# Kernel tuning notes

Measured on AMD Instinct MI355X. Metric: run time of the kernel, lower is better.

The kernel has to match this reference:

```python
import jax, jax.numpy as jnp
import numpy as np

SR = 48000.0
HARMONIC_NUM = 8
DIM = HARMONIC_NUM + 1
SINE_AMP = 0.1
NOISE_STD = 0.003
VOICED_THRESHOLD = 0.0


def setup_inputs() -> dict:
    key = jax.random.key(0)
    k1, k2, k3, k4 = jax.random.split(key, 4)
    B, L, upp = 4, 1000, 512
    Lo = L * upp
    f0 = jax.random.uniform(k1, (B, L), dtype=jnp.float32, minval=80.0, maxval=400.0)
    voiced = jax.random.uniform(k2, (B, L)) > 0.2
    f0 = f0 * voiced.astype(jnp.float32)
    rand_ini = jax.random.uniform(k3, (B, DIM), dtype=jnp.float32)
    noise_randn = jax.random.normal(k4, (B, Lo, DIM), dtype=jnp.float32)
    return {"f0": f0, "rand_ini": rand_ini, "noise_randn": noise_randn, "upp": upp}


def _linear_upsample_align_corners(x, upp):
    # x: (B, L, D) -> (B, L*upp, D), matches F.interpolate(mode='linear', align_corners=True)
    B, L, D = x.shape
    Lo = L * upp
    pos = jnp.arange(Lo, dtype=jnp.float32) * (jnp.float32(L - 1) / jnp.float32(Lo - 1))
    i0 = jnp.clip(jnp.floor(pos).astype(jnp.int32), 0, L - 2)
    frac = (pos - i0.astype(jnp.float32))[None, :, None]
    return x[:, i0, :] * (1.0 - frac) + x[:, i0 + 1, :] * frac


def reference(f0, rand_ini, noise_randn, upp):
    B, L = f0.shape
    Lo = L * upp
    # harmonics: f0, 2*f0, ..., DIM*f0  -> (B, L, DIM)
    f0_buf = f0[:, :, None] * jnp.arange(1, DIM + 1, dtype=f0.dtype)
    rad_values = (f0_buf / SR) % 1.0
    # random initial phase, first harmonic fixed at 0
    ri = rand_ini.at[:, 0].set(0.0)
    rad_values = rad_values.at[:, 0, :].add(ri)
    # cumulative phase at frame rate, scaled and upsampled
    tmp_over_one = jnp.cumsum(rad_values, axis=1) * upp
    tmp_over_one = _linear_upsample_align_corners(tmp_over_one, upp)  # (B, Lo, DIM)
    rad_up = jnp.repeat(rad_values, upp, axis=1)  # nearest upsample (B, Lo, DIM)
    tmp_over_one = tmp_over_one % 1.0
    # detect wrap-around and inject -1 phase shift so cumsum stays consistent
    wrap = (tmp_over_one[:, 1:, :] - tmp_over_one[:, :-1, :]) < 0
    cumsum_shift = jnp.concatenate(
        [jnp.zeros((B, 1, DIM), dtype=f0.dtype), -wrap.astype(f0.dtype)], axis=1
    )
    phase = jnp.cumsum(rad_up + cumsum_shift, axis=1)
    sine_waves = jnp.sin(phase * (2.0 * jnp.pi)) * SINE_AMP
    # voiced/unvoiced mask at frame rate, nearest-upsampled
    uv = (f0 > VOICED_THRESHOLD).astype(f0.dtype)[:, :, None]  # (B, L, 1)
    uv = jnp.repeat(uv, upp, axis=1)  # (B, Lo, 1)
    noise_amp = uv * NOISE_STD + (1.0 - uv) * (SINE_AMP / 3.0)
    noise = noise_amp * noise_randn
    sine_waves = sine_waves * uv + noise
    return sine_waves, uv, noise
```

## Files before the change

### kernel.cpp

```cpp
#include <hip/hip_runtime.h>
#include <math.h>

#define DIM 9
#define SINE_AMP 0.1f
#define NOISE_STD 0.003f

__global__ void __launch_bounds__(64)
phase_scan_kernel(const float* __restrict__ f0,
                  const float* __restrict__ rand_ini,
                  float* __restrict__ rad_out,
                  float* __restrict__ base_out,
                  int B, int L, int upp)
{
    const int bd   = blockIdx.x;
    const int b    = bd / DIM;
    const int d    = bd - b * DIM;
    const int lane = threadIdx.x;
    const float hf = (float)(d + 1);
    const float ri = (d == 0) ? 0.0f : rand_ini[b * DIM + d];

    double carry = 0.0;
    for (int c0 = 0; c0 < L; c0 += 64) {
        const int l = c0 + lane;
        float r = 0.0f;
        if (l < L) {
            float fb = f0[b * L + l] * hf;
            r = fmodf(fb / 48000.0f, 1.0f);
            if (l == 0) r += ri;
        }
        const double rd = (double)r;
        double inc = rd;
        #pragma unroll
        for (int off = 1; off < 64; off <<= 1) {
            double t = __shfl_up(inc, off, 64);
            if (lane >= off) inc += t;
        }
        if (l < L) {
            const double excl = carry + (inc - rd);
            double bf = excl * (double)upp;
            bf -= floor(bf);
            const int idx = (b * L + l) * DIM + d;
            rad_out[idx]  = r;
            base_out[idx] = (float)bf;
        }
        carry += __shfl(inc, 63, 64);
    }
}

template <int UPP>
__global__ void __launch_bounds__(256)
sine_gen_kernel(const float* __restrict__ f0,
                const float* __restrict__ noise_randn,
                const float* __restrict__ rad_arr,
                const float* __restrict__ base_arr,
                float* __restrict__ out_sine,
                float* __restrict__ out_uv,
                float* __restrict__ out_noise,
                int L, int Lo, int upp)
{
    const int b   = blockIdx.y;
    const int LoD = Lo * DIM;
    const int n4  = LoD >> 2;
    const long long boff = (long long)b * LoD;

    const float* __restrict__ nz_b    = noise_randn + boff;
    float* __restrict__       sine_b  = out_sine + boff;
    float* __restrict__       noise_b = out_noise + boff;
    const float* __restrict__ f0_b    = f0 + b * L;
    float* __restrict__       uv_b    = out_uv + (long long)b * Lo;
    const int fbase = b * L * DIM;

    for (int i4 = blockIdx.x * blockDim.x + threadIdx.x; i4 < n4;
         i4 += gridDim.x * blockDim.x) {
        const int i0 = i4 << 2;
        const float4 nr = *(const float4*)(nz_b + i0);
        const float nrk[4] = {nr.x, nr.y, nr.z, nr.w};
        float sv[4], nv[4];
        #pragma unroll
        for (int k = 0; k < 4; ++k) {
            const int rem = i0 + k;
            const int o = rem / DIM;
            const int d = rem - o * DIM;
            int l, j;
            if (UPP > 0) { l = o / UPP; j = o - l * UPP; }
            else         { l = o / upp; j = o - l * upp; }
            const int fidx = fbase + l * DIM + d;
            const float rad  = rad_arr[fidx];
            const float base = base_arr[fidx];
            float ph = base + (float)(j + 1) * rad;
            ph -= floorf(ph);
            float s;
            asm("v_sin_f32 %0, %1" : "=v"(s) : "v"(ph));
            const float f0v  = f0_b[l];
            const float uvf  = (f0v > 0.0f) ? 1.0f : 0.0f;
            const float namp = uvf * NOISE_STD + (1.0f - uvf) * (SINE_AMP / 3.0f);
            const float nzv  = namp * nrk[k];
            nv[k] = nzv;
            sv[k] = s * SINE_AMP * uvf + nzv;
            if (d == 0) uv_b[o] = uvf;
        }
        *(float4*)(sine_b + i0)  = make_float4(sv[0], sv[1], sv[2], sv[3]);
        *(float4*)(noise_b + i0) = make_float4(nv[0], nv[1], nv[2], nv[3]);
    }

    if (blockIdx.x == 0 && threadIdx.x < (LoD & 3)) {
        const int rem = (n4 << 2) + threadIdx.x;
        const int o = rem / DIM;
        const int d = rem - o * DIM;
        int l, j;
        if (UPP > 0) { l = o / UPP; j = o - l * UPP; }
        else         { l = o / upp; j = o - l * upp; }
        const int fidx = fbase + l * DIM + d;
        float ph = base_arr[fidx] + (float)(j + 1) * rad_arr[fidx];
        ph -= floorf(ph);
        float s;
        asm("v_sin_f32 %0, %1" : "=v"(s) : "v"(ph));
        const float f0v  = f0_b[l];
        const float uvf  = (f0v > 0.0f) ? 1.0f : 0.0f;
        const float namp = uvf * NOISE_STD + (1.0f - uvf) * (SINE_AMP / 3.0f);
        const float nzv  = namp * nz_b[rem];
        noise_b[rem] = nzv;
        sine_b[rem]  = s * SINE_AMP * uvf + nzv;
        if (d == 0) uv_b[o] = uvf;
    }
}

extern "C" void kernel_launch(void* const* d_in, const int* in_sizes, int n_in,
                              void* d_out, int out_size, void* d_ws, size_t ws_size,
                              hipStream_t stream)
{
    const float* f0       = (const float*)d_in[0];
    const float* rand_ini = (const float*)d_in[1];
    const float* noise    = (const float*)d_in[2];
    const int B  = in_sizes[1] / DIM;
    const int L  = in_sizes[0] / B;
    const int Lo = in_sizes[2] / (B * DIM);
    const int upp = Lo / L;

    float* out       = (float*)d_out;
    float* out_sine  = out;
    float* out_uv    = out_sine + (long long)B * Lo * DIM;
    float* out_noise = out_uv + (long long)B * Lo;

    float* rad_ws  = (float*)d_ws;
    float* base_ws = rad_ws + (size_t)B * L * DIM;

    phase_scan_kernel<<<dim3(B * DIM), dim3(64), 0, stream>>>(
        f0, rand_ini, rad_ws, base_ws, B, L, upp);

    const int n4 = (Lo * DIM) >> 2;
    int bx = (n4 + 255) / 256;
    if (bx > 1024) bx = 1024;
    dim3 grid(bx, B);
    if (upp == 512) {
        sine_gen_kernel<512><<<grid, dim3(256), 0, stream>>>(
            f0, noise, rad_ws, base_ws, out_sine, out_uv, out_noise, L, Lo, upp);
    } else {
        sine_gen_kernel<0><<<grid, dim3(256), 0, stream>>>(
            f0, noise, rad_ws, base_ws, out_sine, out_uv, out_noise, L, Lo, upp);
    }
}
```

Measured before the change: 53.83 us.

## Pack rad/base into float2 with voicing folded in, nontemporal vector I/O

The scan kernel now writes an interleaved (rad, base) float2 per frame-harmonic and zeroes it for unvoiced frames. It also writes a per-frame noise amplitude, so the generator no longer reads f0 or recomputes the uv mask per element. The sine/noise streams use nontemporal vector loads and stores with unsigned index math. The uv output moves to a separate vectorized loop instead of scattered scalar stores. The aim is fewer gathers and less cache pollution in this bandwidth-bound kernel, at the cost of a second pass for uv and a larger workspace.

Result: slower. 57.29 us (+6.4%).

```diff
diff --git a/kernel.cpp b/kernel.cpp
--- a/kernel.cpp
+++ b/kernel.cpp
@@ -5,11 +5,14 @@
 #define SINE_AMP 0.1f
 #define NOISE_STD 0.003f
 
+typedef float f32x4 __attribute__((ext_vector_type(4)));
+typedef float f32x2 __attribute__((ext_vector_type(2)));
+
 __global__ void __launch_bounds__(64)
 phase_scan_kernel(const float* __restrict__ f0,
                   const float* __restrict__ rand_ini,
-                  float* __restrict__ rad_out,
-                  float* __restrict__ base_out,
+                  f32x2* __restrict__ rb_out,
+                  float* __restrict__ namp_out,
                   int B, int L, int upp)
 {
     const int bd   = blockIdx.x;
@@ -22,10 +25,10 @@
     double carry = 0.0;
     for (int c0 = 0; c0 < L; c0 += 64) {
         const int l = c0 + lane;
-        float r = 0.0f;
+        float r = 0.0f, fv = 0.0f;
         if (l < L) {
-            float fb = f0[b * L + l] * hf;
-            r = fmodf(fb / 48000.0f, 1.0f);
+            fv = f0[b * L + l];
+            r = fmodf(fv * hf / 48000.0f, 1.0f);
             if (l == 0) r += ri;
         }
         const double rd = (double)r;
@@ -39,9 +42,13 @@
             const double excl = carry + (inc - rd);
             double bf = excl * (double)upp;
             bf -= floor(bf);
-            const int idx = (b * L + l) * DIM + d;
-            rad_out[idx]  = r;
-            base_out[idx] = (float)bf;
+            const bool voiced = fv > 0.0f;
+            f32x2 rbv;
+            rbv.x = voiced ? r : 0.0f;
+            rbv.y = voiced ? (float)bf : 0.0f;
+            rb_out[(b * L + l) * DIM + d] = rbv;
+            if (d == 0)
+                namp_out[b * L + l] = voiced ? NOISE_STD : (SINE_AMP / 3.0f);
         }
         carry += __shfl(inc, 63, 64);
     }
@@ -51,77 +58,89 @@
 __global__ void __launch_bounds__(256)
 sine_gen_kernel(const float* __restrict__ f0,
                 const float* __restrict__ noise_randn,
-                const float* __restrict__ rad_arr,
-                const float* __restrict__ base_arr,
+                const f32x2* __restrict__ rb,
+                const float* __restrict__ namp_arr,
                 float* __restrict__ out_sine,
                 float* __restrict__ out_uv,
                 float* __restrict__ out_noise,
                 int L, int Lo, int upp)
 {
+    const unsigned UPPD = (UPP > 0) ? (unsigned)UPP : 1u;
+    const unsigned uppv = (UPP > 0) ? (unsigned)UPP : (unsigned)upp;
+
     const int b   = blockIdx.y;
     const int LoD = Lo * DIM;
-    const int n4  = LoD >> 2;
+    const unsigned n4 = (unsigned)LoD >> 2;
     const long long boff = (long long)b * LoD;
 
-    const float* __restrict__ nz_b    = noise_randn + boff;
-    float* __restrict__       sine_b  = out_sine + boff;
-    float* __restrict__       noise_b = out_noise + boff;
-    const float* __restrict__ f0_b    = f0 + b * L;
-    float* __restrict__       uv_b    = out_uv + (long long)b * Lo;
-    const int fbase = b * L * DIM;
+    const f32x4* __restrict__ nz_b    = (const f32x4*)(noise_randn + boff);
+    f32x4* __restrict__       sine_b  = (f32x4*)(out_sine + boff);
+    f32x4* __restrict__       noise_b = (f32x4*)(out_noise + boff);
+    const float*  __restrict__ f0_b   = f0 + b * L;
+    const float*  __restrict__ namp_b = namp_arr + b * L;
+    const f32x2* __restrict__  rb_b   = rb + b * L * DIM;
 
-    for (int i4 = blockIdx.x * blockDim.x + threadIdx.x; i4 < n4;
-         i4 += gridDim.x * blockDim.x) {
-        const int i0 = i4 << 2;
-        const float4 nr = *(const float4*)(nz_b + i0);
-        const float nrk[4] = {nr.x, nr.y, nr.z, nr.w};
-        float sv[4], nv[4];
+    const unsigned tid    = blockIdx.x * blockDim.x + threadIdx.x;
+    const unsigned stride = gridDim.x * blockDim.x;
+
+    for (unsigned i4 = tid; i4 < n4; i4 += stride) {
+        const unsigned i0 = i4 << 2;
+        const f32x4 nr = __builtin_nontemporal_load(nz_b + i4);
+        f32x4 sv, nv;
         #pragma unroll
         for (int k = 0; k < 4; ++k) {
-            const int rem = i0 + k;
-            const int o = rem / DIM;
-            const int d = rem - o * DIM;
-            int l, j;
-            if (UPP > 0) { l = o / UPP; j = o - l * UPP; }
-            else         { l = o / upp; j = o - l * upp; }
-            const int fidx = fbase + l * DIM + d;
-            const float rad  = rad_arr[fidx];
-            const float base = base_arr[fidx];
-            float ph = base + (float)(j + 1) * rad;
+            const unsigned rem = i0 + (unsigned)k;
+            const unsigned o = rem / 9u;
+            const unsigned d = rem - o * 9u;
+            unsigned l, j;
+            if (UPP > 0) { l = o / UPPD; j = o - l * UPPD; }
+            else         { l = o / (unsigned)upp; j = o - l * (unsigned)upp; }
+            const f32x2 rbv = rb_b[l * 9u + d];
+            float ph = fmaf((float)(j + 1u), rbv.x, rbv.y);
             ph -= floorf(ph);
             float s;
             asm("v_sin_f32 %0, %1" : "=v"(s) : "v"(ph));
-            const float f0v  = f0_b[l];
-            const float uvf  = (f0v > 0.0f) ? 1.0f : 0.0f;
-            const float namp = uvf * NOISE_STD + (1.0f - uvf) * (SINE_AMP / 3.0f);
-            const float nzv  = namp * nrk[k];
+            const float nzv = namp_b[l] * nr[k];
             nv[k] = nzv;
-            sv[k] = s * SINE_AMP * uvf + nzv;
-            if (d == 0) uv_b[o] = uvf;
+            sv[k] = fmaf(s, SINE_AMP, nzv);
         }
-        *(float4*)(sine_b + i0)  = make_float4(sv[0], sv[1], sv[2], sv[3]);
-        *(float4*)(noise_b + i0) = make_float4(nv[0], nv[1], nv[2], nv[3]);
+        __builtin_nontemporal_store(sv, sine_b + i4);
+        __builtin_nontemporal_store(nv, noise_b + i4);
     }
 
-    if (blockIdx.x == 0 && threadIdx.x < (LoD & 3)) {
-        const int rem = (n4 << 2) + threadIdx.x;
-        const int o = rem / DIM;
-        const int d = rem - o * DIM;
-        int l, j;
-        if (UPP > 0) { l = o / UPP; j = o - l * UPP; }
-        else         { l = o / upp; j = o - l * upp; }
-        const int fidx = fbase + l * DIM + d;
-        float ph = base_arr[fidx] + (float)(j + 1) * rad_arr[fidx];
+    f32x4* __restrict__ uv_b4 = (f32x4*)(out_uv + (long long)b * Lo);
+    const unsigned nu4 = (unsigned)Lo >> 2;
+    for (unsigned u4 = tid; u4 < nu4; u4 += stride) {
+        const unsigned o0 = u4 << 2;
+        f32x4 uvv;
+        #pragma unroll
+        for (int k = 0; k < 4; ++k) {
+            const unsigned o = o0 + (unsigned)k;
+            const unsigned l = o / uppv;
+            uvv[k] = (f0_b[l] > 0.0f) ? 1.0f : 0.0f;
+        }
+        __builtin_nontemporal_store(uvv, uv_b4 + u4);
+    }
+
+    if (blockIdx.x == 0 && threadIdx.x < (unsigned)(LoD & 3)) {
+        const unsigned rem = (n4 << 2) + threadIdx.x;
+        const unsigned o = rem / 9u;
+        const unsigned d = rem - o * 9u;
+        const unsigned l = o / uppv;
+        const unsigned j = o - l * uppv;
+        const f32x2 rbv = rb_b[l * 9u + d];
+        float ph = fmaf((float)(j + 1u), rbv.x, rbv.y);
         ph -= floorf(ph);
         float s;
         asm("v_sin_f32 %0, %1" : "=v"(s) : "v"(ph));
-        const float f0v  = f0_b[l];
-        const float uvf  = (f0v > 0.0f) ? 1.0f : 0.0f;
-        const float namp = uvf * NOISE_STD + (1.0f - uvf) * (SINE_AMP / 3.0f);
-        const float nzv  = namp * nz_b[rem];
-        noise_b[rem] = nzv;
-        sine_b[rem]  = s * SINE_AMP * uvf + nzv;
-        if (d == 0) uv_b[o] = uvf;
+        const float nzv = namp_b[l] * ((const float*)nz_b)[rem];
+        ((float*)noise_b)[rem] = nzv;
+        ((float*)sine_b)[rem]  = fmaf(s, SINE_AMP, nzv);
+    }
+    if (blockIdx.x == 0 && threadIdx.x < (unsigned)(Lo & 3)) {
+        const unsigned o = (nu4 << 2) + threadIdx.x;
+        const unsigned l = o / uppv;
+        ((float*)uv_b4)[o] = (f0_b[l] > 0.0f) ? 1.0f : 0.0f;
     }
 }
 
@@ -142,11 +161,11 @@
     float* out_uv    = out_sine + (long long)B * Lo * DIM;
     float* out_noise = out_uv + (long long)B * Lo;
 
-    float* rad_ws  = (float*)d_ws;
-    float* base_ws = rad_ws + (size_t)B * L * DIM;
+    f32x2* rb_ws   = (f32x2*)d_ws;
+    float* namp_ws = (float*)(rb_ws + (size_t)B * L * DIM);
 
     phase_scan_kernel<<<dim3(B * DIM), dim3(64), 0, stream>>>(
-        f0, rand_ini, rad_ws, base_ws, B, L, upp);
+        f0, rand_ini, rb_ws, namp_ws, B, L, upp);
 
     const int n4 = (Lo * DIM) >> 2;
     int bx = (n4 + 255) / 256;
@@ -154,9 +173,9 @@
     dim3 grid(bx, B);
     if (upp == 512) {
         sine_gen_kernel<512><<<grid, dim3(256), 0, stream>>>(
-            f0, noise, rad_ws, base_ws, out_sine, out_uv, out_noise, L, Lo, upp);
+            f0, noise, rb_ws, namp_ws, out_sine, out_uv, out_noise, L, Lo, upp);
     } else {
         sine_gen_kernel<0><<<grid, dim3(256), 0, stream>>>(
-            f0, noise, rad_ws, base_ws, out_sine, out_uv, out_noise, L, Lo, upp);
+            f0, noise, rb_ws, namp_ws, out_sine, out_uv, out_noise, L, Lo, upp);
     }
 }
```
